# Kernel optimization log

Hardware: AMD Instinct MI355X
Metric: run time of the kernel (lower is better)

The kernel has to match this reference:

```python
import jax, jax.numpy as jnp
import numpy as np

N_NODES = 50000
N_EDGES = 150000
N_TRIS = 100000
F = 256
L = 4


def setup_inputs() -> dict:
    key = jax.random.key(0)
    ks = jax.random.split(key, 8)
    x = jax.random.normal(ks[0], (N_EDGES, F), dtype=jnp.float32)
    edge_nodes = jax.random.randint(ks[1], (N_EDGES, 2), 0, N_NODES)
    tri_edges = jax.random.randint(ks[2], (N_TRIS, 3), 0, N_EDGES)
    tri_signs = (jax.random.randint(ks[3], (N_TRIS, 3), 0, 2) * 2 - 1).astype(jnp.int32)
    std = float(np.sqrt(2.0 / (F + F)))  # xavier_uniform-equivalent std
    W0_stack = jax.random.normal(ks[4], (L, F, F), dtype=jnp.float32) * std
    W1_stack = jax.random.normal(ks[5], (L, F, F), dtype=jnp.float32) * std
    W2_stack = jax.random.normal(ks[6], (L, F, F), dtype=jnp.float32) * std
    W0_L = jax.random.normal(ks[7], (F, 1), dtype=jnp.float32) * float(np.sqrt(2.0 / (F + 1)))
    return {"x": x, "W0_stack": W0_stack, "W1_stack": W1_stack, "W2_stack": W2_stack,
            "W0_L": W0_L, "edge_nodes": edge_nodes, "tri_edges": tri_edges, "tri_signs": tri_signs}


def _b1_mm(edge_nodes, y):
    # B1 @ y : [E,F] -> [N,F];  B1[u,e] = -1, B1[v,e] = +1
    u, v = edge_nodes[:, 0], edge_nodes[:, 1]
    out = jnp.zeros((N_NODES, y.shape[1]), y.dtype)
    return out.at[u].add(-y).at[v].add(y)


def _b1t_mm(edge_nodes, z):
    # B1.T @ z : [N,F] -> [E,F]
    return z[edge_nodes[:, 1]] - z[edge_nodes[:, 0]]


def _b2t_mm(tri_edges, signs, y):
    # B2.T @ y : [E,F] -> [T,F]
    return jnp.einsum('tkf,tk->tf', y[tri_edges], signs)


def _b2_mm(tri_edges, signs, w):
    # B2 @ w : [T,F] -> [E,F]
    contrib = w[:, None, :] * signs[:, :, None]  # [T,3,F]
    out = jnp.zeros((N_EDGES, w.shape[1]), w.dtype)
    return out.at[tri_edges.reshape(-1)].add(contrib.reshape(-1, w.shape[1]))


def reference(x, W0_stack, W1_stack, W2_stack, W0_L, edge_nodes, tri_edges, tri_signs):
    signs = tri_signs.astype(x.dtype)
    for i in range(L):
        d2 = _b2_mm(tri_edges, signs, _b2t_mm(tri_edges, signs, x @ W2_stack[i]))
        d1 = x @ W1_stack[i]
        d0 = _b1t_mm(edge_nodes, _b1_mm(edge_nodes, x @ W0_stack[i]))
        x = jax.nn.relu(d2 + d1 + d0)
    return _b1_mm(edge_nodes, x @ W0_L)  # [N_NODES, 1]
```

## Files before the change

kernel.cpp:

```cpp
#include <hip/hip_runtime.h>

#define M_EDGES 150000
#define NN_NODES 50000
#define N_TRIS  100000
#define F 256
#define NLAYERS 4
#define NBM 1172
#define NBM_PAD 1176

typedef __attribute__((ext_vector_type(8))) __bf16 bf16x8;
typedef __attribute__((ext_vector_type(4))) float f32x4;

__device__ inline unsigned short f2bf(float f) {
    unsigned int u = __float_as_uint(f);
    u += 0x7fff + ((u >> 16) & 1);
    return (unsigned short)(u >> 16);
}
__device__ inline float bf2f(unsigned short h) {
    return __uint_as_float(((unsigned int)h) << 16);
}

__device__ inline void async16(const void* g, void* l) {
    __builtin_amdgcn_global_load_lds(
        (const __attribute__((address_space(1))) void*)g,
        (__attribute__((address_space(3))) void*)l, 16, 0, 0);
}

__global__ __launch_bounds__(256) void gemm_mfma(
    const unsigned short* __restrict__ xb,
    const unsigned short* __restrict__ wt,
    unsigned short* __restrict__ y0,
    unsigned short* __restrict__ y1,
    unsigned short* __restrict__ y2)
{
    __shared__ unsigned short As[128 * 32];
    __shared__ unsigned short Bs[128 * 32];

    const int b   = blockIdx.x;
    const int xcd = b & 7;
    const int c   = b >> 3;
    const int bm  = (c / 6) * 8 + xcd;
    const int bn  = c % 6;
    if (bm >= NBM) return;

    const int tid  = threadIdx.x;
    const int bm0  = bm * 128;
    const int wid  = tid >> 6;
    const int lane = tid & 63;
    const int lm   = lane & 15;
    const int lh   = lane >> 4;
    const int wm   = wid >> 1;
    const int wn   = wid & 1;
    const int wbase = tid & ~63;

    f32x4 cacc[4][4];
#pragma unroll
    for (int i = 0; i < 4; i++)
#pragma unroll
        for (int j = 0; j < 4; j++) cacc[i][j] = (f32x4){0.f, 0.f, 0.f, 0.f};

    for (int k0 = 0; k0 < 256; k0 += 32) {
#pragma unroll
        for (int s = 0; s < 2; s++) {
            int i   = s * 256 + tid;
            int row = i >> 2;
            int g   = (i & 3) ^ ((row >> 1) & 3);
            int gr  = bm0 + row;
            if (gr > M_EDGES - 1) gr = M_EDGES - 1;
            async16(xb + (size_t)gr * 256 + k0 + g * 8,
                    As + (size_t)(s * 256 + wbase) * 8);
            int nrow = bn * 128 + row;
            async16(wt + (size_t)nrow * 256 + k0 + g * 8,
                    Bs + (size_t)(s * 256 + wbase) * 8);
        }
        asm volatile("s_waitcnt vmcnt(0)" ::: "memory");
        __syncthreads();

        bf16x8 a[4], bfr[4];
#pragma unroll
        for (int i = 0; i < 4; i++) {
            int rr = wm * 64 + i * 16 + lm;
            a[i] = *(const bf16x8*)(As + rr * 32 + ((lh ^ ((rr >> 1) & 3)) * 8));
        }
#pragma unroll
        for (int j = 0; j < 4; j++) {
            int rr = wn * 64 + j * 16 + lm;
            bfr[j] = *(const bf16x8*)(Bs + rr * 32 + ((lh ^ ((rr >> 1) & 3)) * 8));
        }
#pragma unroll
        for (int i = 0; i < 4; i++)
#pragma unroll
            for (int j = 0; j < 4; j++)
                cacc[i][j] = __builtin_amdgcn_mfma_f32_16x16x32_bf16(a[i], bfr[j], cacc[i][j], 0, 0, 0);
        __syncthreads();
    }

    const int seg = bn >> 1;
    unsigned short* dst = (seg == 0) ? y0 : (seg == 1) ? y1 : y2;
    const int colbase = (bn * 128 + wn * 64) & 255;
#pragma unroll
    for (int i = 0; i < 4; i++) {
#pragma unroll
        for (int r = 0; r < 4; r++) {
            int grow = bm0 + wm * 64 + i * 16 + lh * 4 + r;
            if (grow < M_EDGES) {
#pragma unroll
                for (int j = 0; j < 4; j++) {
                    int col = colbase + j * 16 + lm;
                    dst[(size_t)grow * 256 + col] = f2bf(cacc[i][j][r]);
                }
            }
        }
    }
}

__global__ __launch_bounds__(256) void count_nodes(
    const int* __restrict__ en, int* __restrict__ cnt)
{
    int e = blockIdx.x * 256 + threadIdx.x;
    if (e < M_EDGES) {
        atomicAdd(&cnt[en[2 * e]], 1);
        atomicAdd(&cnt[en[2 * e + 1]], 1);
    }
}

__global__ __launch_bounds__(256) void count_tris(
    const int* __restrict__ te, int* __restrict__ cnt)
{
    int t = blockIdx.x * 256 + threadIdx.x;
    if (t < N_TRIS) {
#pragma unroll
        for (int k = 0; k < 3; k++) atomicAdd(&cnt[te[3 * t + k]], 1);
    }
}

__global__ __launch_bounds__(256) void scan_block(
    const int* __restrict__ cnt, int* __restrict__ off,
    int* __restrict__ partial, int n)
{
    __shared__ int s[256];
    int t = threadIdx.x;
    int gid = blockIdx.x * 256 + t;
    int v = (gid < n) ? cnt[gid] : 0;
    s[t] = v;
    __syncthreads();
    for (int o = 1; o < 256; o <<= 1) {
        int x = (t >= o) ? s[t - o] : 0;
        __syncthreads();
        s[t] += x;
        __syncthreads();
    }
    if (gid < n) off[gid] = s[t] - v;
    if (t == 255) partial[blockIdx.x] = s[255];
}

__global__ __launch_bounds__(1024) void scan_partial(int* __restrict__ partial, int nb)
{
    __shared__ int s[1024];
    int t = threadIdx.x;
    int v = (t < nb) ? partial[t] : 0;
    s[t] = v;
    __syncthreads();
    for (int o = 1; o < 1024; o <<= 1) {
        int x = (t >= o) ? s[t - o] : 0;
        __syncthreads();
        s[t] += x;
        __syncthreads();
    }
    if (t < nb) partial[t] = s[t] - v;
}

__global__ __launch_bounds__(256) void scan_add(
    int* __restrict__ off, int* __restrict__ cursor,
    const int* __restrict__ partial, int n, int total)
{
    int gid = blockIdx.x * 256 + threadIdx.x;
    if (gid == 0) off[n] = total;
    if (gid < n) {
        int o = off[gid] + partial[blockIdx.x];
        off[gid] = o;
        cursor[gid] = o;
    }
}

__global__ __launch_bounds__(256) void fill_nodes(
    const int* __restrict__ en, int* __restrict__ cursor, int* __restrict__ adj)
{
    int e = blockIdx.x * 256 + threadIdx.x;
    if (e < M_EDGES) {
        int u = en[2 * e], v = en[2 * e + 1];
        adj[atomicAdd(&cursor[u], 1)] = (e << 1);
        adj[atomicAdd(&cursor[v], 1)] = (e << 1) | 1;
    }
}

__global__ __launch_bounds__(256) void fill_tris(
    const int* __restrict__ te, const int* __restrict__ ts,
    int* __restrict__ cursor, int* __restrict__ adj)
{
    int t = blockIdx.x * 256 + threadIdx.x;
    if (t < N_TRIS) {
#pragma unroll
        for (int k = 0; k < 3; k++) {
            int e = te[3 * t + k];
            int neg = (ts[3 * t + k] < 0) ? 1 : 0;
            adj[atomicAdd(&cursor[e], 1)] = (t << 1) | neg;
        }
    }
}

#define WT_BLOCKS (N_TRIS / 4)
#define ZN_BLOCKS (NN_NODES / 4)

__global__ __launch_bounds__(256) void zw_fused(
    const unsigned short* __restrict__ y2,
    const int* __restrict__ te,
    const int* __restrict__ ts,
    unsigned short* __restrict__ w,
    const unsigned short* __restrict__ y0,
    const int* __restrict__ noff,
    const int* __restrict__ nadj,
    unsigned short* __restrict__ z)
{
    int lane = threadIdx.x & 63;
    int f = lane * 4;
    if (blockIdx.x < WT_BLOCKS) {
        int t = blockIdx.x * 4 + (threadIdx.x >> 6);
        int e0 = te[3 * t + 0], e1 = te[3 * t + 1], e2 = te[3 * t + 2];
        float s0 = (float)ts[3 * t + 0];
        float s1 = (float)ts[3 * t + 1];
        float s2 = (float)ts[3 * t + 2];
        ushort4 a4 = *(const ushort4*)(y2 + (size_t)e0 * 256 + f);
        ushort4 b4 = *(const ushort4*)(y2 + (size_t)e1 * 256 + f);
        ushort4 d4 = *(const ushort4*)(y2 + (size_t)e2 * 256 + f);
        ushort4 r;
        r.x = f2bf(s0 * bf2f(a4.x) + s1 * bf2f(b4.x) + s2 * bf2f(d4.x));
        r.y = f2bf(s0 * bf2f(a4.y) + s1 * bf2f(b4.y) + s2 * bf2f(d4.y));
        r.z = f2bf(s0 * bf2f(a4.z) + s1 * bf2f(b4.z) + s2 * bf2f(d4.z));
        r.w = f2bf(s0 * bf2f(a4.w) + s1 * bf2f(b4.w) + s2 * bf2f(d4.w));
        *(ushort4*)(w + (size_t)t * 256 + f) = r;
    } else {
        int n = (blockIdx.x - WT_BLOCKS) * 4 + (threadIdx.x >> 6);
        int beg = noff[n], end = noff[n + 1];
        float ax = 0.f, ay = 0.f, az = 0.f, aw = 0.f;
        int i = beg;
        for (; i + 1 < end; i += 2) {
            int ea = nadj[i], eb = nadj[i + 1];
            float sa = (ea & 1) ? 1.f : -1.f;
            float sb = (eb & 1) ? 1.f : -1.f;
            ushort4 va = *(const ushort4*)(y0 + (size_t)(ea >> 1) * 256 + f);
            ushort4 vb = *(const ushort4*)(y0 + (size_t)(eb >> 1) * 256 + f);
            ax += sa * bf2f(va.x) + sb * bf2f(vb.x);
            ay += sa * bf2f(va.y) + sb * bf2f(vb.y);
            az += sa * bf2f(va.z) + sb * bf2f(vb.z);
            aw += sa * bf2f(va.w) + sb * bf2f(vb.w);
        }
        if (i < end) {
            int ea = nadj[i];
            float sa = (ea & 1) ? 1.f : -1.f;
            ushort4 va = *(const ushort4*)(y0 + (size_t)(ea >> 1) * 256 + f);
            ax += sa * bf2f(va.x);
            ay += sa * bf2f(va.y);
            az += sa * bf2f(va.z);
            aw += sa * bf2f(va.w);
        }
        ushort4 r;
        r.x = f2bf(ax); r.y = f2bf(ay); r.z = f2bf(az); r.w = f2bf(aw);
        *(ushort4*)(z + (size_t)n * 256 + f) = r;
    }
}

__global__ __launch_bounds__(256) void relu_fused(
    const unsigned short* __restrict__ y1,
    const unsigned short* __restrict__ w,
    const unsigned short* __restrict__ z,
    const int* __restrict__ en,
    const int* __restrict__ eoff,
    const int* __restrict__ eadj,
    unsigned short* __restrict__ xb)
{
    int e = blockIdx.x * 4 + (threadIdx.x >> 6);
    int lane = threadIdx.x & 63;
    int f = lane * 4;
    int u = en[2 * e], v = en[2 * e + 1];
    int beg = eoff[e], end = eoff[e + 1];
    ushort4 a4 = *(const ushort4*)(y1 + (size_t)e * 256 + f);
    ushort4 zv = *(const ushort4*)(z + (size_t)v * 256 + f);
    ushort4 zu = *(const ushort4*)(z + (size_t)u * 256 + f);
    float sx = bf2f(a4.x) + bf2f(zv.x) - bf2f(zu.x);
    float sy = bf2f(a4.y) + bf2f(zv.y) - bf2f(zu.y);
    float sz = bf2f(a4.z) + bf2f(zv.z) - bf2f(zu.z);
    float sw = bf2f(a4.w) + bf2f(zv.w) - bf2f(zu.w);
    int i = beg;
    for (; i + 1 < end; i += 2) {
        int ta = eadj[i], tb = eadj[i + 1];
        float sa = (ta & 1) ? -1.f : 1.f;
        float sb = (tb & 1) ? -1.f : 1.f;
        ushort4 wa = *(const ushort4*)(w + (size_t)(ta >> 1) * 256 + f);
        ushort4 wbv = *(const ushort4*)(w + (size_t)(tb >> 1) * 256 + f);
        sx += sa * bf2f(wa.x) + sb * bf2f(wbv.x);
        sy += sa * bf2f(wa.y) + sb * bf2f(wbv.y);
        sz += sa * bf2f(wa.z) + sb * bf2f(wbv.z);
        sw += sa * bf2f(wa.w) + sb * bf2f(wbv.w);
    }
    if (i < end) {
        int ta = eadj[i];
        float sa = (ta & 1) ? -1.f : 1.f;
        ushort4 wa = *(const ushort4*)(w + (size_t)(ta >> 1) * 256 + f);
        sx += sa * bf2f(wa.x);
        sy += sa * bf2f(wa.y);
        sz += sa * bf2f(wa.z);
        sw += sa * bf2f(wa.w);
    }
    ushort4 r;
    r.x = f2bf(fmaxf(sx, 0.f));
    r.y = f2bf(fmaxf(sy, 0.f));
    r.z = f2bf(fmaxf(sz, 0.f));
    r.w = f2bf(fmaxf(sw, 0.f));
    *(ushort4*)(xb + (size_t)e * 256 + f) = r;
}

__global__ __launch_bounds__(256) void dotp(
    const unsigned short* __restrict__ xb,
    const float* __restrict__ wl,
    float* __restrict__ p)
{
    int e = blockIdx.x * 4 + (threadIdx.x >> 6);
    int lane = threadIdx.x & 63;
    ushort4 xv = *(const ushort4*)(xb + (size_t)e * 256 + lane * 4);
    float4 wv = *(const float4*)(wl + lane * 4);
    float s = bf2f(xv.x) * wv.x + bf2f(xv.y) * wv.y +
              bf2f(xv.z) * wv.z + bf2f(xv.w) * wv.w;
#pragma unroll
    for (int off = 32; off > 0; off >>= 1)
        s += __shfl_down(s, off, 64);
    if (lane == 0) p[e] = s;
}

__global__ __launch_bounds__(256) void out_nodes(
    const float* __restrict__ p,
    const int* __restrict__ noff,
    const int* __restrict__ nadj,
    float* __restrict__ out)
{
    int n = blockIdx.x * 256 + threadIdx.x;
    if (n >= NN_NODES) return;
    int beg = noff[n], end = noff[n + 1];
    float s = 0.f;
    for (int i = beg; i < end; i++) {
        int ent = nadj[i];
        float sg = (ent & 1) ? 1.f : -1.f;
        s += sg * p[ent >> 1];
    }
    out[n] = s;
}

__global__ __launch_bounds__(256) void cvt_x(
    const float* __restrict__ x, unsigned short* __restrict__ xb)
{
    int idx = blockIdx.x * 256 + threadIdx.x;
    float4 v = *(const float4*)(x + (size_t)idx * 4);
    ushort4 r;
    r.x = f2bf(v.x); r.y = f2bf(v.y); r.z = f2bf(v.z); r.w = f2bf(v.w);
    *(ushort4*)(xb + (size_t)idx * 4) = r;
}

__global__ __launch_bounds__(256) void cvt_w(
    const float* __restrict__ W0, const float* __restrict__ W1,
    const float* __restrict__ W2, unsigned short* __restrict__ wt)
{
    int idx = blockIdx.x * 256 + threadIdx.x;
    int l = idx / (768 * 256);
    int rem = idx - l * (768 * 256);
    int n = rem >> 8;
    int k = rem & 255;
    const float* src;
    int nn;
    if (n < 256)      { src = W0; nn = n; }
    else if (n < 512) { src = W1; nn = n - 256; }
    else              { src = W2; nn = n - 512; }
    wt[idx] = f2bf(src[(size_t)l * 65536 + k * 256 + nn]);
}

extern "C" void kernel_launch(void* const* d_in, const int* in_sizes, int n_in,
                              void* d_out, int out_size, void* d_ws, size_t ws_size,
                              hipStream_t stream)
{
    const float* x0  = (const float*)d_in[0];
    const float* W0s = (const float*)d_in[1];
    const float* W1s = (const float*)d_in[2];
    const float* W2s = (const float*)d_in[3];
    const float* WL  = (const float*)d_in[4];
    const int*   en  = (const int*)d_in[5];
    const int*   te  = (const int*)d_in[6];
    const int*   ts  = (const int*)d_in[7];
    float* out = (float*)d_out;

    const size_t MF = (size_t)M_EDGES * F;
    unsigned short* xb = (unsigned short*)d_ws;
    unsigned short* y0 = xb + MF;
    unsigned short* y1 = y0 + MF;
    unsigned short* y2 = y1 + MF;
    unsigned short* wt = y2 + MF;
    unsigned short* wb = wt + (size_t)4 * 768 * 256;
    unsigned short* zb = wb + (size_t)N_TRIS * 256;
    float* p = (float*)(zb + (size_t)NN_NODES * 256);
    int* noff = (int*)(p + M_EDGES);
    int* ncur = noff + (NN_NODES + 1);
    int* nadj = ncur + NN_NODES;
    int* eoff = nadj + 2 * M_EDGES;
    int* ecur = eoff + (M_EDGES + 1);
    int* eadj = ecur + M_EDGES;
    int* part = eadj + 3 * N_TRIS;

    cvt_w<<<(4 * 768 * 256) / 256, 256, 0, stream>>>(W0s, W1s, W2s, wt);
    cvt_x<<<(int)(MF / 4 / 256), 256, 0, stream>>>(x0, xb);

    const int nbN = (NN_NODES + 255) / 256;
    const int nbE = (M_EDGES + 255) / 256;
    hipMemsetAsync(ncur, 0, NN_NODES * sizeof(int), stream);
    hipMemsetAsync(ecur, 0, M_EDGES * sizeof(int), stream);
    count_nodes<<<nbE, 256, 0, stream>>>(en, ncur);
    count_tris<<<(N_TRIS + 255) / 256, 256, 0, stream>>>(te, ecur);
    scan_block<<<nbN, 256, 0, stream>>>(ncur, noff, part, NN_NODES);
    scan_partial<<<1, 1024, 0, stream>>>(part, nbN);
    scan_add<<<nbN, 256, 0, stream>>>(noff, ncur, part, NN_NODES, 2 * M_EDGES);
    fill_nodes<<<nbE, 256, 0, stream>>>(en, ncur, nadj);
    scan_block<<<nbE, 256, 0, stream>>>(ecur, eoff, part, M_EDGES);
    scan_partial<<<1, 1024, 0, stream>>>(part, nbE);
    scan_add<<<nbE, 256, 0, stream>>>(eoff, ecur, part, M_EDGES, 3 * N_TRIS);
    fill_tris<<<(N_TRIS + 255) / 256, 256, 0, stream>>>(te, ts, ecur, eadj);

    const int gemm_blocks = NBM_PAD * 6;
    for (int l = 0; l < NLAYERS; l++) {
        gemm_mfma<<<gemm_blocks, 256, 0, stream>>>(
            xb, wt + (size_t)l * 768 * 256, y0, y1, y2);
        zw_fused<<<WT_BLOCKS + ZN_BLOCKS, 256, 0, stream>>>(
            y2, te, ts, wb, y0, noff, nadj, zb);
        relu_fused<<<M_EDGES / 4, 256, 0, stream>>>(y1, wb, zb, en, eoff, eadj, xb);
    }

    dotp<<<M_EDGES / 4, 256, 0, stream>>>(xb, WL, p);
    out_nodes<<<(NN_NODES + 255) / 256, 256, 0, stream>>>(p, noff, nadj, out);
}
```

Before: 1.428 ms.

## Aggregate before GEMM to shrink row counts for W0 and W2 products

```diff
diff --git a/kernel.cpp b/kernel.cpp
--- a/kernel.cpp
+++ b/kernel.cpp
@@ -5,8 +5,12 @@
 #define N_TRIS  100000
 #define F 256
 #define NLAYERS 4
-#define NBM 1172
-#define NBM_PAD 1176
+
+#define T0 1172
+#define T1 391
+#define T2 782
+#define NTILES (T0 + T1 + T2)
+#define NT_PAD 2352
 
 typedef __attribute__((ext_vector_type(8))) __bf16 bf16x8;
 typedef __attribute__((ext_vector_type(4))) float f32x4;
@@ -28,23 +32,34 @@
 
 __global__ __launch_bounds__(256) void gemm_mfma(
     const unsigned short* __restrict__ xb,
+    const unsigned short* __restrict__ sb,
+    const unsigned short* __restrict__ qb,
     const unsigned short* __restrict__ wt,
-    unsigned short* __restrict__ y0,
     unsigned short* __restrict__ y1,
-    unsigned short* __restrict__ y2)
+    unsigned short* __restrict__ zb,
+    unsigned short* __restrict__ wb)
 {
     __shared__ unsigned short As[128 * 32];
     __shared__ unsigned short Bs[128 * 32];
 
-    const int b   = blockIdx.x;
-    const int xcd = b & 7;
-    const int c   = b >> 3;
-    const int bm  = (c / 6) * 8 + xcd;
-    const int bn  = c % 6;
-    if (bm >= NBM) return;
+    const int b    = blockIdx.x;
+    const int xcd  = b & 7;
+    const int c    = b >> 3;
+    const int tile = (c >> 1) * 8 + xcd;
+    const int bn   = c & 1;
+    if (tile >= NTILES) return;
+
+    int seg, tloc;
+    if (tile < T0)            { seg = 0; tloc = tile; }
+    else if (tile < T0 + T1)  { seg = 1; tloc = tile - T0; }
+    else                      { seg = 2; tloc = tile - T0 - T1; }
+    const unsigned short* Asrc = (seg == 0) ? xb : (seg == 1) ? sb : qb;
+    const int nrows = (seg == 0) ? M_EDGES : (seg == 1) ? NN_NODES : N_TRIS;
+    const unsigned short* wsel = wt + seg * 65536;
+    unsigned short* dst = (seg == 0) ? y1 : (seg == 1) ? zb : wb;
 
     const int tid  = threadIdx.x;
-    const int bm0  = bm * 128;
+    const int bm0  = tloc * 128;
     const int wid  = tid >> 6;
     const int lane = tid & 63;
     const int lm   = lane & 15;
@@ -66,11 +81,11 @@
             int row = i >> 2;
             int g   = (i & 3) ^ ((row >> 1) & 3);
             int gr  = bm0 + row;
-            if (gr > M_EDGES - 1) gr = M_EDGES - 1;
-            async16(xb + (size_t)gr * 256 + k0 + g * 8,
+            if (gr > nrows - 1) gr = nrows - 1;
+            async16(Asrc + (size_t)gr * 256 + k0 + g * 8,
                     As + (size_t)(s * 256 + wbase) * 8);
             int nrow = bn * 128 + row;
-            async16(wt + (size_t)nrow * 256 + k0 + g * 8,
+            async16(wsel + (size_t)nrow * 256 + k0 + g * 8,
                     Bs + (size_t)(s * 256 + wbase) * 8);
         }
         asm volatile("s_waitcnt vmcnt(0)" ::: "memory");
@@ -91,24 +106,23 @@
         for (int i = 0; i < 4; i++)
 #pragma unroll
             for (int j = 0; j < 4; j++)
-                cacc[i][j] = __builtin_amdgcn_mfma_f32_16x16x32_bf16(a[i], bfr[j], cacc[i][j], 0, 0, 0);
-        __syncthreads();
-    }
-
-    const int seg = bn >> 1;
-    unsigned short* dst = (seg == 0) ? y0 : (seg == 1) ? y1 : y2;
-    const int colbase = (bn * 128 + wn * 64) & 255;
+                cacc[i][j] = __builtin_amdgcn_mfma_f32_16x16x32_bf16(bfr[j], a[i], cacc[i][j], 0, 0, 0);
+        __syncthreads();
+    }
+
 #pragma unroll
     for (int i = 0; i < 4; i++) {
-#pragma unroll
-        for (int r = 0; r < 4; r++) {
-            int grow = bm0 + wm * 64 + i * 16 + lh * 4 + r;
-            if (grow < M_EDGES) {
-#pragma unroll
-                for (int j = 0; j < 4; j++) {
-                    int col = colbase + j * 16 + lm;
-                    dst[(size_t)grow * 256 + col] = f2bf(cacc[i][j][r]);
-                }
+        int grow = bm0 + wm * 64 + i * 16 + lm;
+        if (grow < nrows) {
+#pragma unroll
+            for (int j = 0; j < 4; j++) {
+                int col = bn * 128 + wn * 64 + j * 16 + lh * 4;
+                ushort4 r;
+                r.x = f2bf(cacc[i][j][0]);
+                r.y = f2bf(cacc[i][j][1]);
+                r.z = f2bf(cacc[i][j][2]);
+                r.w = f2bf(cacc[i][j][3]);
+                *(ushort4*)(dst + (size_t)grow * 256 + col) = r;
             }
         }
     }
@@ -209,56 +223,40 @@
     }
 }
 
+#define ZN_BLOCKS (NN_NODES / 4)
 #define WT_BLOCKS (N_TRIS / 4)
-#define ZN_BLOCKS (NN_NODES / 4)
-
-__global__ __launch_bounds__(256) void zw_fused(
-    const unsigned short* __restrict__ y2,
+
+__global__ __launch_bounds__(256) void agg_fused(
+    const unsigned short* __restrict__ xb,
+    const int* __restrict__ noff,
+    const int* __restrict__ nadj,
+    unsigned short* __restrict__ sbuf,
     const int* __restrict__ te,
     const int* __restrict__ ts,
-    unsigned short* __restrict__ w,
-    const unsigned short* __restrict__ y0,
-    const int* __restrict__ noff,
-    const int* __restrict__ nadj,
-    unsigned short* __restrict__ z)
+    unsigned short* __restrict__ qbuf)
 {
     int lane = threadIdx.x & 63;
     int f = lane * 4;
-    if (blockIdx.x < WT_BLOCKS) {
-        int t = blockIdx.x * 4 + (threadIdx.x >> 6);
-        int e0 = te[3 * t + 0], e1 = te[3 * t + 1], e2 = te[3 * t + 2];
-        float s0 = (float)ts[3 * t + 0];
-        float s1 = (float)ts[3 * t + 1];
-        float s2 = (float)ts[3 * t + 2];
-        ushort4 a4 = *(const ushort4*)(y2 + (size_t)e0 * 256 + f);
-        ushort4 b4 = *(const ushort4*)(y2 + (size_t)e1 * 256 + f);
-        ushort4 d4 = *(const ushort4*)(y2 + (size_t)e2 * 256 + f);
-        ushort4 r;
-        r.x = f2bf(s0 * bf2f(a4.x) + s1 * bf2f(b4.x) + s2 * bf2f(d4.x));
-        r.y = f2bf(s0 * bf2f(a4.y) + s1 * bf2f(b4.y) + s2 * bf2f(d4.y));
-        r.z = f2bf(s0 * bf2f(a4.z) + s1 * bf2f(b4.z) + s2 * bf2f(d4.z));
-        r.w = f2bf(s0 * bf2f(a4.w) + s1 * bf2f(b4.w) + s2 * bf2f(d4.w));
-        *(ushort4*)(w + (size_t)t * 256 + f) = r;
-    } else {
-        int n = (blockIdx.x - WT_BLOCKS) * 4 + (threadIdx.x >> 6);
+    if (blockIdx.x < ZN_BLOCKS) {
+        int n = blockIdx.x * 4 + (threadIdx.x >> 6);
         int beg = noff[n], end = noff[n + 1];
         float ax = 0.f, ay = 0.f, az = 0.f, aw = 0.f;
         int i = beg;
         for (; i + 1 < end; i += 2) {
             int ea = nadj[i], eb = nadj[i + 1];
             float sa = (ea & 1) ? 1.f : -1.f;
-            float sb = (eb & 1) ? 1.f : -1.f;
-            ushort4 va = *(const ushort4*)(y0 + (size_t)(ea >> 1) * 256 + f);
-            ushort4 vb = *(const ushort4*)(y0 + (size_t)(eb >> 1) * 256 + f);
-            ax += sa * bf2f(va.x) + sb * bf2f(vb.x);
-            ay += sa * bf2f(va.y) + sb * bf2f(vb.y);
-            az += sa * bf2f(va.z) + sb * bf2f(vb.z);
-            aw += sa * bf2f(va.w) + sb * bf2f(vb.w);
+            float sgb = (eb & 1) ? 1.f : -1.f;
+            ushort4 va = *(const ushort4*)(xb + (size_t)(ea >> 1) * 256 + f);
+            ushort4 vb = *(const ushort4*)(xb + (size_t)(eb >> 1) * 256 + f);
+            ax += sa * bf2f(va.x) + sgb * bf2f(vb.x);
+            ay += sa * bf2f(va.y) + sgb * bf2f(vb.y);
+            az += sa * bf2f(va.z) + sgb * bf2f(vb.z);
+            aw += sa * bf2f(va.w) + sgb * bf2f(vb.w);
         }
         if (i < end) {
             int ea = nadj[i];
             float sa = (ea & 1) ? 1.f : -1.f;
-            ushort4 va = *(const ushort4*)(y0 + (size_t)(ea >> 1) * 256 + f);
+            ushort4 va = *(const ushort4*)(xb + (size_t)(ea >> 1) * 256 + f);
             ax += sa * bf2f(va.x);
             ay += sa * bf2f(va.y);
             az += sa * bf2f(va.z);
@@ -266,7 +264,22 @@
         }
         ushort4 r;
         r.x = f2bf(ax); r.y = f2bf(ay); r.z = f2bf(az); r.w = f2bf(aw);
-        *(ushort4*)(z + (size_t)n * 256 + f) = r;
+        *(ushort4*)(sbuf + (size_t)n * 256 + f) = r;
+    } else {
+        int t = (blockIdx.x - ZN_BLOCKS) * 4 + (threadIdx.x >> 6);
+        int e0 = te[3 * t + 0], e1 = te[3 * t + 1], e2 = te[3 * t + 2];
+        float s0 = (float)ts[3 * t + 0];
+        float s1 = (float)ts[3 * t + 1];
+        float s2 = (float)ts[3 * t + 2];
+        ushort4 a4 = *(const ushort4*)(xb + (size_t)e0 * 256 + f);
+        ushort4 b4 = *(const ushort4*)(xb + (size_t)e1 * 256 + f);
+        ushort4 d4 = *(const ushort4*)(xb + (size_t)e2 * 256 + f);
+        ushort4 r;
+        r.x = f2bf(s0 * bf2f(a4.x) + s1 * bf2f(b4.x) + s2 * bf2f(d4.x));
+        r.y = f2bf(s0 * bf2f(a4.y) + s1 * bf2f(b4.y) + s2 * bf2f(d4.y));
+        r.z = f2bf(s0 * bf2f(a4.z) + s1 * bf2f(b4.z) + s2 * bf2f(d4.z));
+        r.w = f2bf(s0 * bf2f(a4.w) + s1 * bf2f(b4.w) + s2 * bf2f(d4.w));
+        *(ushort4*)(qbuf + (size_t)t * 256 + f) = r;
     }
 }
 
@@ -295,13 +308,13 @@
     for (; i + 1 < end; i += 2) {
         int ta = eadj[i], tb = eadj[i + 1];
         float sa = (ta & 1) ? -1.f : 1.f;
-        float sb = (tb & 1) ? -1.f : 1.f;
+        float sgb = (tb & 1) ? -1.f : 1.f;
         ushort4 wa = *(const ushort4*)(w + (size_t)(ta >> 1) * 256 + f);
         ushort4 wbv = *(const ushort4*)(w + (size_t)(tb >> 1) * 256 + f);
-        sx += sa * bf2f(wa.x) + sb * bf2f(wbv.x);
-        sy += sa * bf2f(wa.y) + sb * bf2f(wbv.y);
-        sz += sa * bf2f(wa.z) + sb * bf2f(wbv.z);
-        sw += sa * bf2f(wa.w) + sb * bf2f(wbv.w);
+        sx += sa * bf2f(wa.x) + sgb * bf2f(wbv.x);
+        sy += sa * bf2f(wa.y) + sgb * bf2f(wbv.y);
+        sz += sa * bf2f(wa.z) + sgb * bf2f(wbv.z);
+        sw += sa * bf2f(wa.w) + sgb * bf2f(wbv.w);
     }
     if (i < end) {
         int ta = eadj[i];
@@ -370,16 +383,13 @@
     const float* __restrict__ W2, unsigned short* __restrict__ wt)
 {
     int idx = blockIdx.x * 256 + threadIdx.x;
-    int l = idx / (768 * 256);
-    int rem = idx - l * (768 * 256);
-    int n = rem >> 8;
+    int l = idx / (3 * 65536);
+    int rem = idx - l * (3 * 65536);
+    int seg = rem >> 16;
+    int n = (rem >> 8) & 255;
     int k = rem & 255;
-    const float* src;
-    int nn;
-    if (n < 256)      { src = W0; nn = n; }
-    else if (n < 512) { src = W1; nn = n - 256; }
-    else              { src = W2; nn = n - 512; }
-    wt[idx] = f2bf(src[(size_t)l * 65536 + k * 256 + nn]);
+    const float* src = (seg == 0) ? W1 : (seg == 1) ? W0 : W2;
+    wt[idx] = f2bf(src[(size_t)l * 65536 + k * 256 + n]);
 }
 
 extern "C" void kernel_launch(void* const* d_in, const int* in_sizes, int n_in,
@@ -398,11 +408,11 @@
 
     const size_t MF = (size_t)M_EDGES * F;
     unsigned short* xb = (unsigned short*)d_ws;
-    unsigned short* y0 = xb + MF;
-    unsigned short* y1 = y0 + MF;
-    unsigned short* y2 = y1 + MF;
-    unsigned short* wt = y2 + MF;
-    unsigned short* wb = wt + (size_t)4 * 768 * 256;
+    unsigned short* y1 = xb + MF;
+    unsigned short* sbuf = y1 + MF;
+    unsigned short* qbuf = sbuf + (size_t)NN_NODES * 256;
+    unsigned short* wt = qbuf + (size_t)N_TRIS * 256;
+    unsigned short* wb = wt + (size_t)4 * 3 * 65536;
     unsigned short* zb = wb + (size_t)N_TRIS * 256;
     float* p = (float*)(zb + (size_t)NN_NODES * 256);
     int* noff = (int*)(p + M_EDGES);
@@ -413,7 +423,7 @@
     int* eadj = ecur + M_EDGES;
     int* part = eadj + 3 * N_TRIS;
 
-    cvt_w<<<(4 * 768 * 256) / 256, 256, 0, stream>>>(W0s, W1s, W2s, wt);
+    cvt_w<<<(4 * 3 * 65536) / 256, 256, 0, stream>>>(W0s, W1s, W2s, wt);
     cvt_x<<<(int)(MF / 4 / 256), 256, 0, stream>>>(x0, xb);
 
     const int nbN = (NN_NODES + 255) / 256;
@@ -431,12 +441,12 @@
     scan_add<<<nbE, 256, 0, stream>>>(eoff, ecur, part, M_EDGES, 3 * N_TRIS);
     fill_tris<<<(N_TRIS + 255) / 256, 256, 0, stream>>>(te, ts, ecur, eadj);
 
-    const int gemm_blocks = NBM_PAD * 6;
+    const int gemm_blocks = NT_PAD * 2;
     for (int l = 0; l < NLAYERS; l++) {
+        agg_fused<<<ZN_BLOCKS + WT_BLOCKS, 256, 0, stream>>>(
+            xb, noff, nadj, sbuf, te, ts, qbuf);
         gemm_mfma<<<gemm_blocks, 256, 0, stream>>>(
-            xb, wt + (size_t)l * 768 * 256, y0, y1, y2);
-        zw_fused<<<WT_BLOCKS + ZN_BLOCKS, 256, 0, stream>>>(
-            y2, te, ts, wb, y0, noff, nadj, zb);
+            xb, sbuf, qbuf, wt + (size_t)l * 3 * 65536, y1, zb, wb);
         relu_fused<<<M_EDGES / 4, 256, 0, stream>>>(y1, wb, zb, en, eoff, eadj, xb);
     }
 
```

After: 1.241 ms. 13.1% less time.
